# Kernel tuning notes

Measured on AMD Instinct MI355X. Metric: run time of the kernel, lower is better.

Reference implementation:

```python
import jax, jax.numpy as jnp
import numpy as np

NF4_LUT = jnp.array([-1.0, -0.6961928009986877, -0.5250730514526367, -0.39491719007492065,
                     -0.28444138169288635, -0.18477343022823334, -0.08820830285549164, 0.0,
                     0.07107656449079514, 0.14263366162776947, 0.22430233657360077,
                     0.3203405737876892, 0.4407068192958832, 0.5905631184577942,
                     0.796090841293335, 1.0], dtype=jnp.float32)

BLOCK_SIZE = 64
OUT_FEATURES = 11008
IN_FEATURES = 4096


def dequantize_nf4(packed, absmax, out_shape):
    # packed: (O, I//2) int codes 0..255; absmax: (O, num_blocks)
    higher = packed // 16
    lower = packed % 16
    unpacked = jnp.stack([lower, higher], axis=-1).reshape(out_shape)  # (O, I)
    dequant = NF4_LUT[unpacked]  # LUT gather -> fp32 (O, I)
    O, I = out_shape
    # block-wise absmax scale
    dequant = (dequant.reshape(O, I // BLOCK_SIZE, BLOCK_SIZE) * absmax[:, :, None]).reshape(O, I)
    return dequant


def setup_inputs() -> dict:
    key = jax.random.key(0)
    k1, k2, k3, k4 = jax.random.split(key, 4)
    x = jax.random.normal(k1, (4, 2048, IN_FEATURES), dtype=jnp.float32)
    weight = jax.random.randint(k2, (OUT_FEATURES, IN_FEATURES // 2), 0, 256, dtype=jnp.int32)
    absmax = jax.random.uniform(k3, (OUT_FEATURES, IN_FEATURES // BLOCK_SIZE), dtype=jnp.float32)
    bias = jax.random.normal(k4, (OUT_FEATURES,), dtype=jnp.float32)
    return {"x": x, "weight": weight, "absmax": absmax, "bias": bias}


def reference(x, weight, absmax, bias):
    w = dequantize_nf4(weight, absmax, (OUT_FEATURES, IN_FEATURES))  # (O, I)
    # F.linear: y = x @ w.T + bias
    return jnp.einsum('bsi,oi->bso', x, w) + bias
```

## Files before the change

### kernel.cpp

```cpp
#include <hip/hip_runtime.h>

#define IN_F 4096
#define OUT_F 11008

typedef __attribute__((ext_vector_type(8))) short bf16x8;
typedef __attribute__((ext_vector_type(4))) float f32x4;
typedef __attribute__((ext_vector_type(4))) unsigned short us4;
typedef __attribute__((ext_vector_type(8))) unsigned short us8;

__device__ __forceinline__ unsigned short f2bf(float f) {
  unsigned int u = __float_as_uint(f);
  u += 0x7FFFu + ((u >> 16) & 1u);
  return (unsigned short)(u >> 16);
}

__global__ __launch_bounds__(256) void cvt_x(const float* __restrict__ X,
                                             unsigned short* __restrict__ Xb, int n8) {
  for (int i = blockIdx.x * blockDim.x + threadIdx.x; i < n8;
       i += gridDim.x * blockDim.x) {
    const float4 a = reinterpret_cast<const float4*>(X)[2 * i];
    const float4 b = reinterpret_cast<const float4*>(X)[2 * i + 1];
    us8 h;
    h[0] = f2bf(a.x); h[1] = f2bf(a.y); h[2] = f2bf(a.z); h[3] = f2bf(a.w);
    h[4] = f2bf(b.x); h[5] = f2bf(b.y); h[6] = f2bf(b.z); h[7] = f2bf(b.w);
    reinterpret_cast<us8*>(Xb)[i] = h;
  }
}

__global__ __launch_bounds__(256) void dequant_w(const int* __restrict__ Wp,
                                                 const float* __restrict__ Amax,
                                                 unsigned short* __restrict__ Wb, int n4) {
  __shared__ float lutS[16];
  if (threadIdx.x < 16) {
    const float lut[16] = {-1.0f, -0.6961928009986877f, -0.5250730514526367f,
        -0.39491719007492065f, -0.28444138169288635f, -0.18477343022823334f,
        -0.08820830285549164f, 0.0f, 0.07107656449079514f, 0.14263366162776947f,
        0.22430233657360077f, 0.3203405737876892f, 0.4407068192958832f,
        0.5905631184577942f, 0.796090841293335f, 1.0f};
    lutS[threadIdx.x] = lut[threadIdx.x];
  }
  __syncthreads();
  for (int i = blockIdx.x * blockDim.x + threadIdx.x; i < n4;
       i += gridDim.x * blockDim.x) {
    const int j = i * 4;
    const int row = j >> 11;
    const int coli = j & 2047;
    const float am = Amax[row * (IN_F / 64) + (coli >> 5)];
    const int4 pk = reinterpret_cast<const int4*>(Wp)[i];
    us8 h; int c;
    c = pk.x & 255; h[0] = f2bf(lutS[c & 15] * am); h[1] = f2bf(lutS[c >> 4] * am);
    c = pk.y & 255; h[2] = f2bf(lutS[c & 15] * am); h[3] = f2bf(lutS[c >> 4] * am);
    c = pk.z & 255; h[4] = f2bf(lutS[c & 15] * am); h[5] = f2bf(lutS[c >> 4] * am);
    c = pk.w & 255; h[6] = f2bf(lutS[c & 15] * am); h[7] = f2bf(lutS[c >> 4] * am);
    reinterpret_cast<us8*>(Wb)[i] = h;
  }
}

#define MF(a, b, c) __builtin_amdgcn_mfma_f32_16x16x32_bf16(a, b, c, 0, 0, 0)
#define GLDS(src, dst) __builtin_amdgcn_global_load_lds( \
    (const __attribute__((address_space(1))) void*)(src), \
    (__attribute__((address_space(3))) void*)(dst), 16, 0, 0)
#define FENCE asm volatile("" ::: "memory")
#define BAR do { FENCE; __builtin_amdgcn_s_barrier(); FENCE; } while (0)
#define VM6 asm volatile("s_waitcnt vmcnt(6)" ::: "memory")
#define VM0 asm volatile("s_waitcnt vmcnt(0)" ::: "memory")
#define VMNOP do {} while (0)
#define P1 __builtin_amdgcn_s_setprio(1)
#define P0 __builtin_amdgcn_s_setprio(0)

__global__ __launch_bounds__(512, 2) void gemm256(
    const unsigned short* __restrict__ A,
    const unsigned short* __restrict__ B,
    const float* __restrict__ Bias, float* __restrict__ Out, int M) {
  extern __shared__ unsigned short sm[];
  char* const smc = (char*)sm;

  const int tid = threadIdx.x;
  const int l = tid & 63;
  const int wid = tid >> 6;

  const int Mb = M / 256;
  const int Nb = OUT_F / 256;

  const int bps = 16 * Nb;
  const int pxc = bps >> 3;
  const int i6 = (int)blockIdx.x % bps;
  const int sup = (int)blockIdx.x / bps;
  const int k = (i6 & 7) * pxc + (i6 >> 3);
  const int m0 = (sup * 16 + (k & 15)) * 256;
  const int n0 = (k >> 4) * 256;

  const int lv = (l & 15) * 64 + (((l >> 4) ^ ((l >> 1) & 3)) * 16);
  const int aLane = (wid >> 2) * 8192 + lv;
  const int bLane = 32768 + (wid & 3) * 4096 + lv;

  const int rq = tid >> 2;
  const int cs = (tid & 3) ^ ((tid >> 3) & 3);
  const unsigned short* gAs = A + (size_t)(m0 + rq) * IN_F + cs * 8;
  const unsigned short* gBs = B + (size_t)(n0 + rq) * IN_F + cs * 8;

#define SA(t, kh) do { \
    unsigned short* d_ = sm + (size_t)((((t) & 1) * 4096) + (kh) * 1024 + wid * 64) * 8; \
    const unsigned short* s_ = gAs + (size_t)(t) * 64 + (kh) * 32; \
    GLDS(s_, d_); GLDS(s_ + 524288, d_ + 4096); } while (0)
#define SB(t, kh) do { \
    unsigned short* d_ = sm + (size_t)((((t) & 1) * 4096) + 2048 + (kh) * 1024 + wid * 64) * 8; \
    const unsigned short* s_ = gBs + (size_t)(t) * 64 + (kh) * 32; \
    GLDS(s_, d_); GLDS(s_ + 524288, d_ + 4096); } while (0)

#define RD_A(kh) do { const char* p_ = LAb + (kh) * 16384; \
    a0 = *(const bf16x8*)(p_);        a1 = *(const bf16x8*)(p_ + 1024); \
    a2 = *(const bf16x8*)(p_ + 2048); a3 = *(const bf16x8*)(p_ + 3072); \
    a4 = *(const bf16x8*)(p_ + 4096); a5 = *(const bf16x8*)(p_ + 5120); \
    a6 = *(const bf16x8*)(p_ + 6144); a7 = *(const bf16x8*)(p_ + 7168); } while (0)
#define RD_B01(kh) do { const char* p_ = LBb + (kh) * 16384; \
    b0 = *(const bf16x8*)(p_); b1 = *(const bf16x8*)(p_ + 1024); } while (0)
#define RD_B23(kh) do { const char* p_ = LBb + (kh) * 16384 + 2048; \
    b2 = *(const bf16x8*)(p_); b3 = *(const bf16x8*)(p_ + 1024); } while (0)

#define MM16_01(B0, B1) do { \
    acc[0][0]=MF(a0,B0,acc[0][0]); acc[0][1]=MF(a0,B1,acc[0][1]); \
    acc[1][0]=MF(a1,B0,acc[1][0]); acc[1][1]=MF(a1,B1,acc[1][1]); \
    acc[2][0]=MF(a2,B0,acc[2][0]); acc[2][1]=MF(a2,B1,acc[2][1]); \
    acc[3][0]=MF(a3,B0,acc[3][0]); acc[3][1]=MF(a3,B1,acc[3][1]); \
    acc[4][0]=MF(a4,B0,acc[4][0]); acc[4][1]=MF(a4,B1,acc[4][1]); \
    acc[5][0]=MF(a5,B0,acc[5][0]); acc[5][1]=MF(a5,B1,acc[5][1]); \
    acc[6][0]=MF(a6,B0,acc[6][0]); acc[6][1]=MF(a6,B1,acc[6][1]); \
    acc[7][0]=MF(a7,B0,acc[7][0]); acc[7][1]=MF(a7,B1,acc[7][1]); } while (0)
#define MM16_23(B2, B3) do { \
    acc[0][2]=MF(a0,B2,acc[0][2]); acc[0][3]=MF(a0,B3,acc[0][3]); \
    acc[1][2]=MF(a1,B2,acc[1][2]); acc[1][3]=MF(a1,B3,acc[1][3]); \
    acc[2][2]=MF(a2,B2,acc[2][2]); acc[2][3]=MF(a2,B3,acc[2][3]); \
    acc[3][2]=MF(a3,B2,acc[3][2]); acc[3][3]=MF(a3,B3,acc[3][3]); \
    acc[4][2]=MF(a4,B2,acc[4][2]); acc[4][3]=MF(a4,B3,acc[4][3]); \
    acc[5][2]=MF(a5,B2,acc[5][2]); acc[5][3]=MF(a5,B3,acc[5][3]); \
    acc[6][2]=MF(a6,B2,acc[6][2]); acc[6][3]=MF(a6,B3,acc[6][3]); \
    acc[7][2]=MF(a7,B2,acc[7][2]); acc[7][3]=MF(a7,B3,acc[7][3]); } while (0)

#define KTILE(T, S1, S2, VMW) do { \
    const char* LAb = smc + (((T) & 1) << 16) + aLane; \
    const char* LBb = smc + (((T) & 1) << 16) + bLane; \
    bf16x8 a0, a1, a2, a3, a4, a5, a6, a7, b0, b1, b2, b3; \
    RD_A(0); RD_B01(0); \
    if (S1) SB((T) + 1, 1); \
    BAR; P1; MM16_01(b0, b1); P0; BAR; \
    RD_B23(0); \
    if (S2) SA((T) + 2, 0); \
    BAR; P1; MM16_23(b2, b3); P0; BAR; \
    RD_A(1); RD_B01(1); \
    if (S2) SB((T) + 2, 0); \
    BAR; P1; MM16_01(b0, b1); P0; BAR; \
    RD_B23(1); \
    if (S2) SA((T) + 2, 1); \
    VMW; \
    BAR; P1; MM16_23(b2, b3); P0; BAR; \
  } while (0)

  f32x4 acc[8][4];
#pragma unroll
  for (int i = 0; i < 8; ++i)
#pragma unroll
    for (int j = 0; j < 4; ++j) acc[i][j] = {0.f, 0.f, 0.f, 0.f};

  SA(0, 0); SB(0, 0); SA(0, 1); SB(0, 1); SA(1, 0); SB(1, 0); SA(1, 1);
  VM6;
  BAR;

  for (int T = 0; T < 62; ++T) { KTILE(T, 1, 1, VM6); }
  KTILE(62, 1, 0, VM0);
  KTILE(63, 0, 0, VMNOP);

  const int crow = m0 + (wid >> 2) * 128 + ((l >> 4) << 2);
  const int ccol = n0 + (wid & 3) * 64 + (l & 15);
#pragma unroll
  for (int nf = 0; nf < 4; ++nf) {
    const float bv = Bias[ccol + nf * 16];
#pragma unroll
    for (int f = 0; f < 8; ++f)
#pragma unroll
      for (int rg = 0; rg < 4; ++rg)
        Out[(size_t)(crow + f * 16 + rg) * OUT_F + ccol + nf * 16] = acc[f][nf][rg] + bv;
  }
}

__global__ __launch_bounds__(256, 2) void nf4_gemm_fused(
    const float* __restrict__ X, const int* __restrict__ Wp,
    const float* __restrict__ Amax, const float* __restrict__ Bias,
    float* __restrict__ Out, int M) {
  __shared__ unsigned short As[128 * 64];
  __shared__ unsigned short Bs[128 * 64];
  __shared__ float lutS[16];

  const int t = threadIdx.x;
  const int l = t & 63;
  const int wid = t >> 6;

  if (t < 16) {
    const float lut[16] = {-1.0f, -0.6961928009986877f, -0.5250730514526367f,
        -0.39491719007492065f, -0.28444138169288635f, -0.18477343022823334f,
        -0.08820830285549164f, 0.0f, 0.07107656449079514f, 0.14263366162776947f,
        0.22430233657360077f, 0.3203405737876892f, 0.4407068192958832f,
        0.5905631184577942f, 0.796090841293335f, 1.0f};
    lutS[t] = lut[t];
  }

  const int ntile = OUT_F / 128;
  const int m0 = (blockIdx.x / ntile) * 128;
  const int n0 = (blockIdx.x % ntile) * 128;

  const int ar = t >> 4;
  const int ac4 = t & 15;
  const int br = t >> 3;
  const int bg = t & 7;
  const int wm = (wid >> 1) * 64;
  const int wn = (wid & 1) * 64;

  f32x4 acc[4][4];
#pragma unroll
  for (int i = 0; i < 4; ++i)
#pragma unroll
    for (int j = 0; j < 4; ++j) acc[i][j] = {0.f, 0.f, 0.f, 0.f};

  __syncthreads();

  for (int k0 = 0; k0 < IN_F; k0 += 64) {
#pragma unroll
    for (int p = 0; p < 8; ++p) {
      const int r = p * 16 + ar;
      const float4 v = *reinterpret_cast<const float4*>(
          X + (size_t)(m0 + r) * IN_F + k0 + ac4 * 4);
      us4 h;
      h[0] = f2bf(v.x); h[1] = f2bf(v.y); h[2] = f2bf(v.z); h[3] = f2bf(v.w);
      const int byte = r * 128 + ((ac4 * 8) ^ ((r & 7) << 4));
      *reinterpret_cast<us4*>(reinterpret_cast<char*>(As) + byte) = h;
    }
#pragma unroll
    for (int p = 0; p < 4; ++p) {
      const int r = p * 32 + br;
      const float amv = Amax[(size_t)(n0 + r) * (IN_F / 64) + (k0 >> 6)];
      const int4 pk = *reinterpret_cast<const int4*>(
          Wp + (size_t)(n0 + r) * (IN_F / 2) + (k0 >> 1) + bg * 4);
      us8 h;
      {
        int c;
        c = pk.x & 255; h[0] = f2bf(lutS[c & 15] * amv); h[1] = f2bf(lutS[c >> 4] * amv);
        c = pk.y & 255; h[2] = f2bf(lutS[c & 15] * amv); h[3] = f2bf(lutS[c >> 4] * amv);
        c = pk.z & 255; h[4] = f2bf(lutS[c & 15] * amv); h[5] = f2bf(lutS[c >> 4] * amv);
        c = pk.w & 255; h[6] = f2bf(lutS[c & 15] * amv); h[7] = f2bf(lutS[c >> 4] * amv);
      }
      const int byte = r * 128 + ((bg * 16) ^ ((r & 7) << 4));
      *reinterpret_cast<us8*>(reinterpret_cast<char*>(Bs) + byte) = h;
    }
    __syncthreads();

#pragma unroll
    for (int kk = 0; kk < 64; kk += 32) {
      bf16x8 af[4], bfv[4];
      const int kb = (kk + ((l >> 4) << 3)) * 2;
#pragma unroll
      for (int i = 0; i < 4; ++i) {
        const int row = wm + i * 16 + (l & 15);
        af[i] = *reinterpret_cast<const bf16x8*>(
            reinterpret_cast<const char*>(As) + row * 128 + (kb ^ ((row & 7) << 4)));
      }
#pragma unroll
      for (int j = 0; j < 4; ++j) {
        const int row = wn + j * 16 + (l & 15);
        bfv[j] = *reinterpret_cast<const bf16x8*>(
            reinterpret_cast<const char*>(Bs) + row * 128 + (kb ^ ((row & 7) << 4)));
      }
#pragma unroll
      for (int i = 0; i < 4; ++i)
#pragma unroll
        for (int j = 0; j < 4; ++j)
          acc[i][j] = __builtin_amdgcn_mfma_f32_16x16x32_bf16(af[i], bfv[j], acc[i][j], 0, 0, 0);
    }
    __syncthreads();
  }

  const int crow0 = m0 + wm + ((l >> 4) << 2);
  const int ccol0 = n0 + wn + (l & 15);
#pragma unroll
  for (int j = 0; j < 4; ++j) {
    const float bv = Bias[ccol0 + j * 16];
#pragma unroll
    for (int i = 0; i < 4; ++i)
#pragma unroll
      for (int rg = 0; rg < 4; ++rg)
        Out[(size_t)(crow0 + i * 16 + rg) * OUT_F + ccol0 + j * 16] = acc[i][j][rg] + bv;
  }
}

extern "C" void kernel_launch(void* const* d_in, const int* in_sizes, int n_in,
                              void* d_out, int out_size, void* d_ws, size_t ws_size,
                              hipStream_t stream) {
  const float* X = (const float*)d_in[0];
  const int* Wp = (const int*)d_in[1];
  const float* Amax = (const float*)d_in[2];
  const float* Bias = (const float*)d_in[3];
  float* Out = (float*)d_out;

  const int M = in_sizes[0] / IN_F;
  const size_t needX = (size_t)M * IN_F * 2;
  const size_t needW = (size_t)OUT_F * IN_F * 2;
  const int grid256 = (M / 256) * (OUT_F / 256);

  if (ws_size >= needX + needW && (M % 4096) == 0) {
    unsigned short* Xb = (unsigned short*)d_ws;
    unsigned short* Wb = Xb + (size_t)M * IN_F;
    (void)hipFuncSetAttribute(reinterpret_cast<const void*>(gemm256),
                              hipFuncAttributeMaxDynamicSharedMemorySize, 131072);
    cvt_x<<<2048, 256, 0, stream>>>(X, Xb, M * (IN_F / 8));
    dequant_w<<<2048, 256, 0, stream>>>(Wp, Amax, Wb, OUT_F * (IN_F / 8));
    gemm256<<<grid256, 512, 131072, stream>>>(Xb, Wb, Bias, Out, M);
  } else {
    const int grid = (M / 128) * (OUT_F / 128);
    nf4_gemm_fused<<<grid, 256, 0, stream>>>(X, Wp, Amax, Bias, Out, M);
  }
}
```

Measured before the change: 794.3 us.

## Simplify GEMM main loop to single-stage prefetch with full-tile fragment loads

Result: slower. 866.6 us (+9.1%).

```diff
diff --git a/kernel.cpp b/kernel.cpp
--- a/kernel.cpp
+++ b/kernel.cpp
@@ -62,9 +62,7 @@
     (__attribute__((address_space(3))) void*)(dst), 16, 0, 0)
 #define FENCE asm volatile("" ::: "memory")
 #define BAR do { FENCE; __builtin_amdgcn_s_barrier(); FENCE; } while (0)
-#define VM6 asm volatile("s_waitcnt vmcnt(6)" ::: "memory")
 #define VM0 asm volatile("s_waitcnt vmcnt(0)" ::: "memory")
-#define VMNOP do {} while (0)
 #define P1 __builtin_amdgcn_s_setprio(1)
 #define P0 __builtin_amdgcn_s_setprio(0)
 
@@ -79,7 +77,6 @@
   const int l = tid & 63;
   const int wid = tid >> 6;
 
-  const int Mb = M / 256;
   const int Nb = OUT_F / 256;
 
   const int bps = 16 * Nb;
@@ -106,54 +103,53 @@
 #define SB(t, kh) do { \
     unsigned short* d_ = sm + (size_t)((((t) & 1) * 4096) + 2048 + (kh) * 1024 + wid * 64) * 8; \
     const unsigned short* s_ = gBs + (size_t)(t) * 64 + (kh) * 32; \
+    GLDS(s_, d_); GLDS(s_ + 4096, d_ + 4096); } while (0)
+#undef SB
+#define SB(t, kh) do { \
+    unsigned short* d_ = sm + (size_t)((((t) & 1) * 4096) + 2048 + (kh) * 1024 + wid * 64) * 8; \
+    const unsigned short* s_ = gBs + (size_t)(t) * 64 + (kh) * 32; \
     GLDS(s_, d_); GLDS(s_ + 524288, d_ + 4096); } while (0)
 
-#define RD_A(kh) do { const char* p_ = LAb + (kh) * 16384; \
-    a0 = *(const bf16x8*)(p_);        a1 = *(const bf16x8*)(p_ + 1024); \
-    a2 = *(const bf16x8*)(p_ + 2048); a3 = *(const bf16x8*)(p_ + 3072); \
-    a4 = *(const bf16x8*)(p_ + 4096); a5 = *(const bf16x8*)(p_ + 5120); \
-    a6 = *(const bf16x8*)(p_ + 6144); a7 = *(const bf16x8*)(p_ + 7168); } while (0)
-#define RD_B01(kh) do { const char* p_ = LBb + (kh) * 16384; \
-    b0 = *(const bf16x8*)(p_); b1 = *(const bf16x8*)(p_ + 1024); } while (0)
-#define RD_B23(kh) do { const char* p_ = LBb + (kh) * 16384 + 2048; \
-    b2 = *(const bf16x8*)(p_); b3 = *(const bf16x8*)(p_ + 1024); } while (0)
-
-#define MM16_01(B0, B1) do { \
-    acc[0][0]=MF(a0,B0,acc[0][0]); acc[0][1]=MF(a0,B1,acc[0][1]); \
-    acc[1][0]=MF(a1,B0,acc[1][0]); acc[1][1]=MF(a1,B1,acc[1][1]); \
-    acc[2][0]=MF(a2,B0,acc[2][0]); acc[2][1]=MF(a2,B1,acc[2][1]); \
-    acc[3][0]=MF(a3,B0,acc[3][0]); acc[3][1]=MF(a3,B1,acc[3][1]); \
-    acc[4][0]=MF(a4,B0,acc[4][0]); acc[4][1]=MF(a4,B1,acc[4][1]); \
-    acc[5][0]=MF(a5,B0,acc[5][0]); acc[5][1]=MF(a5,B1,acc[5][1]); \
-    acc[6][0]=MF(a6,B0,acc[6][0]); acc[6][1]=MF(a6,B1,acc[6][1]); \
-    acc[7][0]=MF(a7,B0,acc[7][0]); acc[7][1]=MF(a7,B1,acc[7][1]); } while (0)
-#define MM16_23(B2, B3) do { \
-    acc[0][2]=MF(a0,B2,acc[0][2]); acc[0][3]=MF(a0,B3,acc[0][3]); \
-    acc[1][2]=MF(a1,B2,acc[1][2]); acc[1][3]=MF(a1,B3,acc[1][3]); \
-    acc[2][2]=MF(a2,B2,acc[2][2]); acc[2][3]=MF(a2,B3,acc[2][3]); \
-    acc[3][2]=MF(a3,B2,acc[3][2]); acc[3][3]=MF(a3,B3,acc[3][3]); \
-    acc[4][2]=MF(a4,B2,acc[4][2]); acc[4][3]=MF(a4,B3,acc[4][3]); \
-    acc[5][2]=MF(a5,B2,acc[5][2]); acc[5][3]=MF(a5,B3,acc[5][3]); \
-    acc[6][2]=MF(a6,B2,acc[6][2]); acc[6][3]=MF(a6,B3,acc[6][3]); \
-    acc[7][2]=MF(a7,B2,acc[7][2]); acc[7][3]=MF(a7,B3,acc[7][3]); } while (0)
-
-#define KTILE(T, S1, S2, VMW) do { \
+#define MM32(AA0, AA1, AA2, AA3, AA4, AA5, AA6, AA7, BB0, BB1, BB2, BB3) do { \
+    acc[0][0]=MF(AA0,BB0,acc[0][0]); acc[0][1]=MF(AA0,BB1,acc[0][1]); \
+    acc[0][2]=MF(AA0,BB2,acc[0][2]); acc[0][3]=MF(AA0,BB3,acc[0][3]); \
+    acc[1][0]=MF(AA1,BB0,acc[1][0]); acc[1][1]=MF(AA1,BB1,acc[1][1]); \
+    acc[1][2]=MF(AA1,BB2,acc[1][2]); acc[1][3]=MF(AA1,BB3,acc[1][3]); \
+    acc[2][0]=MF(AA2,BB0,acc[2][0]); acc[2][1]=MF(AA2,BB1,acc[2][1]); \
+    acc[2][2]=MF(AA2,BB2,acc[2][2]); acc[2][3]=MF(AA2,BB3,acc[2][3]); \
+    acc[3][0]=MF(AA3,BB0,acc[3][0]); acc[3][1]=MF(AA3,BB1,acc[3][1]); \
+    acc[3][2]=MF(AA3,BB2,acc[3][2]); acc[3][3]=MF(AA3,BB3,acc[3][3]); \
+    acc[4][0]=MF(AA4,BB0,acc[4][0]); acc[4][1]=MF(AA4,BB1,acc[4][1]); \
+    acc[4][2]=MF(AA4,BB2,acc[4][2]); acc[4][3]=MF(AA4,BB3,acc[4][3]); \
+    acc[5][0]=MF(AA5,BB0,acc[5][0]); acc[5][1]=MF(AA5,BB1,acc[5][1]); \
+    acc[5][2]=MF(AA5,BB2,acc[5][2]); acc[5][3]=MF(AA5,BB3,acc[5][3]); \
+    acc[6][0]=MF(AA6,BB0,acc[6][0]); acc[6][1]=MF(AA6,BB1,acc[6][1]); \
+    acc[6][2]=MF(AA6,BB2,acc[6][2]); acc[6][3]=MF(AA6,BB3,acc[6][3]); \
+    acc[7][0]=MF(AA7,BB0,acc[7][0]); acc[7][1]=MF(AA7,BB1,acc[7][1]); \
+    acc[7][2]=MF(AA7,BB2,acc[7][2]); acc[7][3]=MF(AA7,BB3,acc[7][3]); } while (0)
+
+#define KTILE(T, STG) do { \
+    VM0; \
+    BAR; \
     const char* LAb = smc + (((T) & 1) << 16) + aLane; \
     const char* LBb = smc + (((T) & 1) << 16) + bLane; \
-    bf16x8 a0, a1, a2, a3, a4, a5, a6, a7, b0, b1, b2, b3; \
-    RD_A(0); RD_B01(0); \
-    if (S1) SB((T) + 1, 1); \
-    BAR; P1; MM16_01(b0, b1); P0; BAR; \
-    RD_B23(0); \
-    if (S2) SA((T) + 2, 0); \
-    BAR; P1; MM16_23(b2, b3); P0; BAR; \
-    RD_A(1); RD_B01(1); \
-    if (S2) SB((T) + 2, 0); \
-    BAR; P1; MM16_01(b0, b1); P0; BAR; \
-    RD_B23(1); \
-    if (S2) SA((T) + 2, 1); \
-    VMW; \
-    BAR; P1; MM16_23(b2, b3); P0; BAR; \
+    bf16x8 x0, x1, x2, x3, x4, x5, x6, x7, y0, y1, y2, y3; \
+    bf16x8 u0, u1, u2, u3, u4, u5, u6, u7, v0, v1, v2, v3; \
+    y0 = *(const bf16x8*)(LBb);        y1 = *(const bf16x8*)(LBb + 1024); \
+    y2 = *(const bf16x8*)(LBb + 2048); y3 = *(const bf16x8*)(LBb + 3072); \
+    x0 = *(const bf16x8*)(LAb);        x1 = *(const bf16x8*)(LAb + 1024); \
+    x2 = *(const bf16x8*)(LAb + 2048); x3 = *(const bf16x8*)(LAb + 3072); \
+    x4 = *(const bf16x8*)(LAb + 4096); x5 = *(const bf16x8*)(LAb + 5120); \
+    x6 = *(const bf16x8*)(LAb + 6144); x7 = *(const bf16x8*)(LAb + 7168); \
+    v0 = *(const bf16x8*)(LBb + 16384);        v1 = *(const bf16x8*)(LBb + 16384 + 1024); \
+    v2 = *(const bf16x8*)(LBb + 16384 + 2048); v3 = *(const bf16x8*)(LBb + 16384 + 3072); \
+    u0 = *(const bf16x8*)(LAb + 16384);        u1 = *(const bf16x8*)(LAb + 16384 + 1024); \
+    u2 = *(const bf16x8*)(LAb + 16384 + 2048); u3 = *(const bf16x8*)(LAb + 16384 + 3072); \
+    u4 = *(const bf16x8*)(LAb + 16384 + 4096); u5 = *(const bf16x8*)(LAb + 16384 + 5120); \
+    u6 = *(const bf16x8*)(LAb + 16384 + 6144); u7 = *(const bf16x8*)(LAb + 16384 + 7168); \
+    if (STG) { SA((T) + 1, 0); SB((T) + 1, 0); SA((T) + 1, 1); SB((T) + 1, 1); } \
+    P1; MM32(x0, x1, x2, x3, x4, x5, x6, x7, y0, y1, y2, y3); P0; \
+    P1; MM32(u0, u1, u2, u3, u4, u5, u6, u7, v0, v1, v2, v3); P0; \
   } while (0)
 
   f32x4 acc[8][4];
@@ -162,13 +158,10 @@
 #pragma unroll
     for (int j = 0; j < 4; ++j) acc[i][j] = {0.f, 0.f, 0.f, 0.f};
 
-  SA(0, 0); SB(0, 0); SA(0, 1); SB(0, 1); SA(1, 0); SB(1, 0); SA(1, 1);
-  VM6;
-  BAR;
-
-  for (int T = 0; T < 62; ++T) { KTILE(T, 1, 1, VM6); }
-  KTILE(62, 1, 0, VM0);
-  KTILE(63, 0, 0, VMNOP);
+  SA(0, 0); SB(0, 0); SA(0, 1); SB(0, 1);
+
+  for (int T = 0; T < 63; ++T) { KTILE(T, 1); }
+  KTILE(63, 0);
 
   const int crow = m0 + (wid >> 2) * 128 + ((l >> 4) << 2);
   const int ccol = n0 + (wid & 3) * 64 + (l & 15);
```
